# Optimization experiments

Hardware: AMD Instinct MI355X
Metric: run time of the kernel (lower is better)

The kernel has to match this reference:

```python
import jax, jax.numpy as jnp
import numpy as np

N_HEAD = 16
L_PARAM = 2  # module's L; min block = 2**L


def _build_sets(T, Lp):
    sets = []
    L = 2 ** Lp
    while L <= T:
        for i in range(T // L):
            sets.append((i * L, (i + 1) * L - 1))
        L *= 2
    return np.asarray(sets, dtype=np.int32)  # [nsets, 2]


def _get_slice(x_cum, l_idx, r_idx):
    # x_cum: [B, nh, T, hs]; returns cumulative-sum slice sums for each (l, r)
    r = x_cum[:, :, r_idx, :]
    l = x_cum[:, :, l_idx - 1, :] * (l_idx >= 1)[None, None, :, None]
    return r - l


def setup_inputs() -> dict:
    key = jax.random.key(0)
    k1, k2, k3 = jax.random.split(key, 3)
    B, T, C = 2, 2048, 1024
    x = jax.random.normal(k1, (B, T, C), dtype=jnp.float32)
    W_attn = jax.random.normal(k2, (3 * C, C), dtype=jnp.float32) * 0.02
    W_proj = jax.random.normal(k3, (C, C), dtype=jnp.float32) * 0.02
    return {"x": x, "W_attn": W_attn, "W_proj": W_proj}


def reference(x, W_attn, W_proj):
    B, T, C = x.shape
    nh, hs = N_HEAD, C // N_HEAD
    scale = 1.0 / np.sqrt(hs).astype(np.float32)

    qkv = x @ W_attn.T  # [B, T, 3C]
    q, k, v = jnp.split(qkv, 3, axis=2)
    q = q.reshape(B, T, nh, hs).transpose(0, 2, 1, 3)  # [B, nh, T, hs]
    k = k.reshape(B, T, nh, hs).transpose(0, 2, 1, 3)
    v = v.reshape(B, T, nh, hs).transpose(0, 2, 1, 3)

    # phi is identity, so q_phi = q, k_phi = k
    k_cum = jnp.cumsum(k, axis=2)
    v_cum = jnp.cumsum(v, axis=2)

    sets = _build_sets(T, L_PARAM)  # static, [nsets, 2]
    l_idx = jnp.asarray(sets[:, 0])
    r_idx = jnp.asarray(sets[:, 1])

    K = _get_slice(k_cum, l_idx, r_idx)  # [B, nh, nsets, hs]
    V = _get_slice(v_cum, l_idx, r_idx)

    t = jnp.arange(T)
    mask = t[:, None] >= r_idx[None, :]  # [T, nsets]

    att_logits = jnp.einsum('bhtd,bhsd->bhts', q, K) * scale
    att_logits = jnp.where(mask[None, None], att_logits, -jnp.inf)

    # tail term: remaining t % 2**L + 1 keys for each query
    Lmin = 2 ** L_PARAM
    tail_len = t % Lmin + 1
    l_tail = t - tail_len + 1
    K_tail = _get_slice(k_cum, l_tail, t)  # [B, nh, T, hs]
    V_tail = _get_slice(v_cum, l_tail, t)
    att_tail = jnp.sum(q * K_tail, axis=-1) * scale  # [B, nh, T]

    logits = jnp.concatenate([att_logits, att_tail[..., None]], axis=-1)
    att = jax.nn.softmax(logits, axis=-1)

    out = jnp.einsum('bhts,bhsd->bhtd', att[..., :-1], V) + att[..., -1:] * V_tail
    out = out.transpose(0, 2, 1, 3).reshape(B, T, C)
    return out @ W_proj.T
```

## Files before the change

kernel.cpp:

```cpp
#include <hip/hip_runtime.h>

typedef _Float16 f16x8 __attribute__((ext_vector_type(8)));
typedef unsigned short u16x8 __attribute__((ext_vector_type(8)));
typedef float f32x4  __attribute__((ext_vector_type(4)));
typedef unsigned short u16;

#define T_SEQ 2048
#define C_DIM 1024
#define NH 16
#define HS 64
#define S_SETS 1023
#define S_PAD 1024
#define SCALE 0.125f
#define NEG_BIG -1e30f

#define GLB(p) ((const __attribute__((address_space(1))) void*)(p))
#define LDS(p) ((__attribute__((address_space(3))) void*)(p))

__device__ __forceinline__ u16 f2h(float f) {
    _Float16 h = (_Float16)f;
    return __builtin_bit_cast(unsigned short, h);
}
__device__ __forceinline__ float h2f(u16 u) {
    _Float16 h = __builtin_bit_cast(_Float16, u);
    return (float)h;
}
__device__ __forceinline__ f32x4 mfmah(f16x8 a, f16x8 b, f32x4 c) {
    return __builtin_amdgcn_mfma_f32_16x16x32_f16(a, b, c, 0, 0, 0);
}

__global__ __launch_bounds__(256) void conv_f16(const float* __restrict__ in,
                                                u16* __restrict__ out, int n4) {
    int i = blockIdx.x * 256 + threadIdx.x;
    if (i >= n4) return;
    float4 f = ((const float4*)in)[i];
    ushort4 o;
    o.x = f2h(f.x); o.y = f2h(f.y); o.z = f2h(f.z); o.w = f2h(f.w);
    ((ushort4*)out)[i] = o;
}

__global__ __launch_bounds__(256) void gemm_qkv16(const u16* __restrict__ x16,
                                                  const u16* __restrict__ wa16,
                                                  u16* __restrict__ q16,
                                                  u16* __restrict__ k16,
                                                  u16* __restrict__ v16) {
    __shared__ u16 As[128 * 32];
    __shared__ u16 Bs[128 * 32];
    int tid = threadIdx.x, wv = tid >> 6, lane = tid & 63;
    int lm = lane & 15, quad = lane >> 4;
    int mt = blockIdx.x / 24, nt = blockIdx.x % 24;
    int wm = wv >> 1, wn = wv & 1;
    int m_off = wm * 64, n_off = wn * 64;

    const u16* gsrc;
    u16* ldst;
    int half = wv & 1;
    if (wv < 2) { gsrc = x16  + (size_t)(mt * 128 + half * 64) * C_DIM; ldst = As + half * 64 * 32; }
    else        { gsrc = wa16 + (size_t)(nt * 128 + half * 64) * C_DIM; ldst = Bs + half * 64 * 32; }
    int srow = lane >> 2, scol = (lane & 3) * 8;

    f32x4 acc[4][4];
    #pragma unroll
    for (int i = 0; i < 4; ++i)
        #pragma unroll
        for (int j = 0; j < 4; ++j) acc[i][j] = (f32x4){0.f, 0.f, 0.f, 0.f};

    for (int k0 = 0; k0 < C_DIM; k0 += 32) {
        __syncthreads();
        #pragma unroll
        for (int i = 0; i < 4; ++i) {
            int row = i * 16 + srow;
            __builtin_amdgcn_global_load_lds(
                GLB(gsrc + (size_t)row * C_DIM + k0 + scol),
                LDS(ldst + i * 512), 16, 0, 0);
        }
        __syncthreads();
        f16x8 af[4], bf[4];
        #pragma unroll
        for (int i = 0; i < 4; ++i) {
            af[i] = *(const f16x8*)(As + (m_off + i * 16 + lm) * 32 + quad * 8);
            bf[i] = *(const f16x8*)(Bs + (n_off + i * 16 + lm) * 32 + quad * 8);
        }
        #pragma unroll
        for (int mi = 0; mi < 4; ++mi)
            #pragma unroll
            for (int ni = 0; ni < 4; ++ni)
                acc[mi][ni] = mfmah(af[mi], bf[ni], acc[mi][ni]);
    }

    #pragma unroll
    for (int mi = 0; mi < 4; ++mi)
        #pragma unroll
        for (int ni = 0; ni < 4; ++ni) {
            int n = nt * 128 + n_off + ni * 16 + lm;
            int which = n >> 10, h = (n >> 6) & 15, d = n & 63;
            #pragma unroll
            for (int reg = 0; reg < 4; ++reg) {
                int m = mt * 128 + m_off + mi * 16 + quad * 4 + reg;
                int b_ = m >> 11, t = m & 2047;
                size_t oi = (((size_t)(b_ * NH + h)) * T_SEQ + t) * HS + d;
                float val = acc[mi][ni][reg];
                if (which == 0)      q16[oi] = f2h(val * SCALE);
                else if (which == 1) k16[oi] = f2h(val);
                else                 v16[oi] = f2h(val);
            }
        }
}

__global__ __launch_bounds__(256) void set_sums(const u16* __restrict__ k16,
                                                const u16* __restrict__ v16,
                                                u16* __restrict__ K16,
                                                u16* __restrict__ VT16) {
    int bh  = blockIdx.x;
    int src = blockIdx.y >> 2;
    int dc  = blockIdx.y & 3;
    int tid = threadIdx.x;
    __shared__ float lv0[512 * 16];
    __shared__ float lv1[256 * 16];
    const u16* sp = src ? v16 : k16;
    u16* op = src ? VT16 : K16;
    int dbase = dc * 16;
    for (int idx = tid; idx < 512 * 16; idx += 256) {
        int sg = idx >> 4, dd = idx & 15, d = dbase + dd;
        const u16* p = sp + ((size_t)bh * T_SEQ + sg * 4) * HS + d;
        float s = h2f(p[0]) + h2f(p[HS]) + h2f(p[2 * HS]) + h2f(p[3 * HS]);
        lv0[sg * 16 + dd] = s;
        size_t o = src ? ((size_t)bh * HS + d) * S_PAD + sg
                       : ((size_t)bh * S_PAD + sg) * HS + d;
        op[o] = f2h(s);
    }
    __syncthreads();
    int nsets = 256, offset = 512, lvl = 1;
    while (nsets >= 1) {
        float* sbuf = (lvl & 1) ? lv0 : lv1;
        float* dbuf = (lvl & 1) ? lv1 : lv0;
        for (int idx = tid; idx < nsets * 16; idx += 256) {
            int i = idx >> 4, dd = idx & 15, d = dbase + dd;
            float s = sbuf[(2 * i) * 16 + dd] + sbuf[(2 * i + 1) * 16 + dd];
            dbuf[i * 16 + dd] = s;
            int so = offset + i;
            size_t o = src ? ((size_t)bh * HS + d) * S_PAD + so
                           : ((size_t)bh * S_PAD + so) * HS + d;
            op[o] = f2h(s);
        }
        __syncthreads();
        offset += nsets; nsets >>= 1; lvl++;
    }
}

__global__ __launch_bounds__(256) void attn_flash16(const u16* __restrict__ q16,
                                                    const u16* __restrict__ k16,
                                                    const u16* __restrict__ v16,
                                                    const u16* __restrict__ K16,
                                                    const u16* __restrict__ VT16,
                                                    u16* __restrict__ att16) {
    int bh = blockIdx.y;
    int tid = threadIdx.x, wv = tid >> 6, lane = tid & 63;
    int lm = lane & 15, quad = lane >> 4;
    int tgrp = (wv < 2) ? (32 * blockIdx.x) : (2016 - 32 * blockIdx.x);
    int t0w = tgrp + (wv & 1) * 16;
    int twmax = t0w + 15;

    __shared__ u16 Ks[128 * 64];
    __shared__ u16 Pbuf[4][16 * 136];
    __shared__ float ptl[4][16];

    const u16* qg = q16 + ((size_t)bh * T_SEQ + t0w + lm) * HS;
    f16x8 a0 = *(const f16x8*)(qg + quad * 8);
    f16x8 a1 = *(const f16x8*)(qg + 32 + quad * 8);

    f32x4 O[4];
    #pragma unroll
    for (int i = 0; i < 4; ++i) O[i] = (f32x4){0.f, 0.f, 0.f, 0.f};
    f32x4 mrun = (f32x4){NEG_BIG, NEG_BIG, NEG_BIG, NEG_BIG};
    f32x4 lrun = (f32x4){0.f, 0.f, 0.f, 0.f};

    u16* Pw = &Pbuf[wv][0];
    const u16* vb = VT16 + (size_t)bh * HS * S_PAD;

    for (int c = 0; c < 8; ++c) {
        int s0 = c * 128;
        __syncthreads();
        {
            int row = tid >> 1, gb = (tid & 1) * 4, rx = row & 7;
            const u16* gk = K16 + ((size_t)bh * S_PAD + s0 + row) * HS;
            u16* dst = Ks + row * 64;
            #pragma unroll
            for (int uu = 0; uu < 4; ++uu) {
                int g = gb + uu;
                *(u16x8*)(dst + ((g ^ rx) << 3)) = *(const u16x8*)(gk + g * 8);
            }
        }
        __syncthreads();

        unsigned flags = 0;
        f32x4 lt[8];
        #pragma unroll
        for (int st = 0; st < 8; ++st) {
            int s = s0 + st * 16 + lm;
            bool sval = (s < S_SETS);
            int r = 0;
            if (sval) {
                int e = S_SETS - s;
                int l = __clz(e) - 22;
                int i0 = s - (1024 - (1024 >> l));
                r = (i0 + 1) * (4 << l) - 1;
            }
            unsigned long long bal = __ballot(sval && (r <= twmax));
            if (bal) {
                flags |= 1u << st;
                int sl = st * 16 + lm, sx = sl & 7;
                f16x8 b0 = *(const f16x8*)(Ks + sl * 64 + ((quad ^ sx) << 3));
                f16x8 b1 = *(const f16x8*)(Ks + sl * 64 + (((4 + quad) ^ sx) << 3));
                f32x4 a = (f32x4){0.f, 0.f, 0.f, 0.f};
                a = mfmah(a0, b0, a);
                a = mfmah(a1, b1, a);
                #pragma unroll
                for (int reg = 0; reg < 4; ++reg) {
                    int t = t0w + quad * 4 + reg;
                    lt[st][reg] = (sval && t >= r) ? a[reg] : NEG_BIG;
                }
            }
        }
        if (!flags) continue;

        f32x4 mc = (f32x4){NEG_BIG, NEG_BIG, NEG_BIG, NEG_BIG};
        #pragma unroll
        for (int st = 0; st < 8; ++st)
            if ((flags >> st) & 1u)
                #pragma unroll
                for (int reg = 0; reg < 4; ++reg) mc[reg] = fmaxf(mc[reg], lt[st][reg]);
        #pragma unroll
        for (int off = 1; off < 16; off <<= 1)
            #pragma unroll
            for (int reg = 0; reg < 4; ++reg)
                mc[reg] = fmaxf(mc[reg], __shfl_xor(mc[reg], off));
        f32x4 mnew, alpha, rs = (f32x4){0.f, 0.f, 0.f, 0.f};
        #pragma unroll
        for (int reg = 0; reg < 4; ++reg) {
            mnew[reg] = fmaxf(mrun[reg], mc[reg]);
            alpha[reg] = __expf(mrun[reg] - mnew[reg]);
        }
        #pragma unroll
        for (int st = 0; st < 8; ++st) {
            if ((flags >> st) & 1u) {
                #pragma unroll
                for (int reg = 0; reg < 4; ++reg) {
                    float lv = lt[st][reg];
                    float p = (lv > -5e29f) ? __expf(lv - mnew[reg]) : 0.f;
                    rs[reg] += p;
                    Pw[(quad * 4 + reg) * 136 + st * 16 + lm] = f2h(p);
                }
            } else {
                #pragma unroll
                for (int reg = 0; reg < 4; ++reg)
                    Pw[(quad * 4 + reg) * 136 + st * 16 + lm] = 0;
            }
        }
        #pragma unroll
        for (int off = 1; off < 16; off <<= 1)
            #pragma unroll
            for (int reg = 0; reg < 4; ++reg) rs[reg] += __shfl_xor(rs[reg], off);
        #pragma unroll
        for (int reg = 0; reg < 4; ++reg) {
            lrun[reg] = lrun[reg] * alpha[reg] + rs[reg];
            mrun[reg] = mnew[reg];
        }
        #pragma unroll
        for (int dt = 0; dt < 4; ++dt)
            #pragma unroll
            for (int reg = 0; reg < 4; ++reg) O[dt][reg] *= alpha[reg];

        #pragma unroll
        for (int kc = 0; kc < 4; ++kc) {
            if (!((flags >> (2 * kc)) & 3u)) continue;
            f16x8 afr = *(const f16x8*)(Pw + lm * 136 + kc * 32 + quad * 8);
            #pragma unroll
            for (int dt = 0; dt < 4; ++dt) {
                size_t vo = (size_t)(dt * 16 + lm) * S_PAD + s0 + kc * 32 + quad * 8;
                f16x8 bv = *(const f16x8*)(vb + vo);
                O[dt] = mfmah(afr, bv, O[dt]);
            }
        }
    }

    {
        int rqr = lane >> 2, prt = lane & 3;
        int tt = t0w + rqr;
        int lenr = (tt & 3) + 1;
        float ktv[16];
        #pragma unroll
        for (int dd = 0; dd < 16; ++dd) ktv[dd] = 0.f;
        for (int j = 0; j < lenr; ++j) {
            const u16* kp = k16 + ((size_t)bh * T_SEQ + tt - j) * HS + prt * 16;
            #pragma unroll
            for (int dd = 0; dd < 16; ++dd) ktv[dd] += h2f(kp[dd]);
        }
        const u16* tq = q16 + ((size_t)bh * T_SEQ + tt) * HS + prt * 16;
        float tlp = 0.f;
        #pragma unroll
        for (int dd = 0; dd < 16; ++dd) tlp += h2f(tq[dd]) * ktv[dd];
        tlp += __shfl_xor(tlp, 1);
        tlp += __shfl_xor(tlp, 2);
        if (prt == 0) ptl[wv][rqr] = tlp;
    }
    __syncthreads();

    int b_ = bh >> 4, h_ = bh & 15;
    #pragma unroll
    for (int reg = 0; reg < 4; ++reg) {
        int row = quad * 4 + reg;
        int t = t0w + row;
        float tl = ptl[wv][row];
        float mfin = fmaxf(mrun[reg], tl);
        float pt = __expf(tl - mfin);
        float af = __expf(mrun[reg] - mfin);
        float inv = 1.0f / (lrun[reg] * af + pt);
        int len = (t & 3) + 1;
        #pragma unroll
        for (int dt = 0; dt < 4; ++dt) {
            int d = dt * 16 + lm;
            const u16* vp = v16 + ((size_t)bh * T_SEQ + t) * HS + d;
            float vt = 0.f;
            for (int j = 0; j < len; ++j) vt += h2f(vp[-(j * HS)]);
            float val = (O[dt][reg] * af + pt * vt) * inv;
            att16[((size_t)(b_ * T_SEQ + t)) * C_DIM + h_ * HS + d] = f2h(val);
        }
    }
}

__global__ __launch_bounds__(256) void gemm_proj16(const u16* __restrict__ a_,
                                                   const u16* __restrict__ w,
                                                   float* __restrict__ out) {
    __shared__ u16 As[128 * 32];
    __shared__ u16 Bs[128 * 32];
    int tid = threadIdx.x, wv = tid >> 6, lane = tid & 63;
    int lm = lane & 15, quad = lane >> 4;
    int mt = blockIdx.x >> 3, nt = blockIdx.x & 7;
    int wm = wv >> 1, wn = wv & 1;
    int m_off = wm * 64, n_off = wn * 64;

    const u16* gsrc;
    u16* ldst;
    int half = wv & 1;
    if (wv < 2) { gsrc = a_ + (size_t)(mt * 128 + half * 64) * C_DIM; ldst = As + half * 64 * 32; }
    else        { gsrc = w  + (size_t)(nt * 128 + half * 64) * C_DIM; ldst = Bs + half * 64 * 32; }
    int srow = lane >> 2, scol = (lane & 3) * 8;

    f32x4 acc[4][4];
    #pragma unroll
    for (int i = 0; i < 4; ++i)
        #pragma unroll
        for (int j = 0; j < 4; ++j) acc[i][j] = (f32x4){0.f, 0.f, 0.f, 0.f};

    for (int k0 = 0; k0 < C_DIM; k0 += 32) {
        __syncthreads();
        #pragma unroll
        for (int i = 0; i < 4; ++i) {
            int row = i * 16 + srow;
            __builtin_amdgcn_global_load_lds(
                GLB(gsrc + (size_t)row * C_DIM + k0 + scol),
                LDS(ldst + i * 512), 16, 0, 0);
        }
        __syncthreads();
        f16x8 af[4], bf[4];
        #pragma unroll
        for (int i = 0; i < 4; ++i) {
            af[i] = *(const f16x8*)(As + (m_off + i * 16 + lm) * 32 + quad * 8);
            bf[i] = *(const f16x8*)(Bs + (n_off + i * 16 + lm) * 32 + quad * 8);
        }
        #pragma unroll
        for (int mi = 0; mi < 4; ++mi)
            #pragma unroll
            for (int ni = 0; ni < 4; ++ni)
                acc[mi][ni] = mfmah(af[mi], bf[ni], acc[mi][ni]);
    }

    #pragma unroll
    for (int mi = 0; mi < 4; ++mi)
        #pragma unroll
        for (int ni = 0; ni < 4; ++ni) {
            int n = nt * 128 + n_off + ni * 16 + lm;
            #pragma unroll
            for (int reg = 0; reg < 4; ++reg) {
                int m = mt * 128 + m_off + mi * 16 + quad * 4 + reg;
                out[(size_t)m * C_DIM + n] = acc[mi][ni][reg];
            }
        }
}

extern "C" void kernel_launch(void* const* d_in, const int* in_sizes, int n_in,
                              void* d_out, int out_size, void* d_ws, size_t ws_size,
                              hipStream_t stream) {
    const float* x     = (const float*)d_in[0];
    const float* Wattn = (const float*)d_in[1];
    const float* Wproj = (const float*)d_in[2];
    float* out = (float*)d_out;
    char* ws = (char*)d_ws;
    u16* x16   = (u16*)(ws + 0);
    u16* wa16  = (u16*)(ws + 8388608);
    u16* wp16  = (u16*)(ws + 14680064);
    u16* q16   = (u16*)(ws + 16777216);
    u16* k16   = (u16*)(ws + 25165824);
    u16* v16   = (u16*)(ws + 33554432);
    u16* K16   = (u16*)(ws + 41943040);
    u16* VT16  = (u16*)(ws + 46137344);
    u16* att16 = (u16*)(ws + 50331648);

    hipLaunchKernelGGL(conv_f16, dim3(4096), dim3(256), 0, stream, x, x16, 1048576);
    hipLaunchKernelGGL(conv_f16, dim3(3072), dim3(256), 0, stream, Wattn, wa16, 786432);
    hipLaunchKernelGGL(conv_f16, dim3(1024), dim3(256), 0, stream, Wproj, wp16, 262144);
    hipLaunchKernelGGL(gemm_qkv16, dim3(768), dim3(256), 0, stream, x16, wa16, q16, k16, v16);
    hipLaunchKernelGGL(set_sums, dim3(32, 8), dim3(256), 0, stream, k16, v16, K16, VT16);
    hipLaunchKernelGGL(attn_flash16, dim3(32, 32), dim3(256), 0, stream,
                       q16, k16, v16, K16, VT16, att16);
    hipLaunchKernelGGL(gemm_proj16, dim3(256), dim3(256), 0, stream, att16, wp16, out);
}
```

Before: 234.1 us.

## Split attention over set halves with LSE combine kernel and direct K loads

Splits the attention kernel's 1024 sets into two halves across a new grid dimension, each writing a normalized partial output and a log-sum-exp. A new combine kernel merges the two partials with the tail term. The per-chunk K tile staged in LDS is replaced by direct global loads, which removes two block barriers per chunk. Launch bounds now request 6 blocks per CU, and workspace buffers are reused. This is meant to raise parallelism and occupancy, at the cost of an extra kernel launch, extra partial-output traffic, and wasted work on the upper half where many queries see no valid sets.

Measured after the change: 346.4 us. 1.48x slower.

```diff
diff --git a/kernel.cpp b/kernel.cpp
--- a/kernel.cpp
+++ b/kernel.cpp
@@ -120,6 +120,12 @@
     const u16* sp = src ? v16 : k16;
     u16* op = src ? VT16 : K16;
     int dbase = dc * 16;
+    if (tid < 16) {
+        int d = dbase + tid;
+        size_t o = src ? ((size_t)bh * HS + d) * S_PAD + 1023
+                       : ((size_t)bh * S_PAD + 1023) * HS + d;
+        op[o] = 0;
+    }
     for (int idx = tid; idx < 512 * 16; idx += 256) {
         int sg = idx >> 4, dd = idx & 15, d = dbase + dd;
         const u16* p = sp + ((size_t)bh * T_SEQ + sg * 4) * HS + d;
@@ -148,22 +154,20 @@
     }
 }
 
-__global__ __launch_bounds__(256) void attn_flash16(const u16* __restrict__ q16,
-                                                    const u16* __restrict__ k16,
-                                                    const u16* __restrict__ v16,
-                                                    const u16* __restrict__ K16,
-                                                    const u16* __restrict__ VT16,
-                                                    u16* __restrict__ att16) {
+__global__ __launch_bounds__(256, 6) void attn_flash16(const u16* __restrict__ q16,
+                                                       const u16* __restrict__ K16,
+                                                       const u16* __restrict__ VT16,
+                                                       u16* __restrict__ Opart,
+                                                       float* __restrict__ LSEpart) {
     int bh = blockIdx.y;
+    int half = blockIdx.z;
     int tid = threadIdx.x, wv = tid >> 6, lane = tid & 63;
     int lm = lane & 15, quad = lane >> 4;
     int tgrp = (wv < 2) ? (32 * blockIdx.x) : (2016 - 32 * blockIdx.x);
     int t0w = tgrp + (wv & 1) * 16;
     int twmax = t0w + 15;
 
-    __shared__ u16 Ks[128 * 64];
-    __shared__ u16 Pbuf[4][16 * 136];
-    __shared__ float ptl[4][16];
+    __shared__ u16 Pbuf[4][16 * 72];
 
     const u16* qg = q16 + ((size_t)bh * T_SEQ + t0w + lm) * HS;
     f16x8 a0 = *(const f16x8*)(qg + quad * 8);
@@ -176,27 +180,16 @@
     f32x4 lrun = (f32x4){0.f, 0.f, 0.f, 0.f};
 
     u16* Pw = &Pbuf[wv][0];
-    const u16* vb = VT16 + (size_t)bh * HS * S_PAD;
+    const u16* vb  = VT16 + (size_t)bh * HS * S_PAD;
+    const u16* kbh = K16  + (size_t)bh * S_PAD * HS;
 
     for (int c = 0; c < 8; ++c) {
-        int s0 = c * 128;
-        __syncthreads();
-        {
-            int row = tid >> 1, gb = (tid & 1) * 4, rx = row & 7;
-            const u16* gk = K16 + ((size_t)bh * S_PAD + s0 + row) * HS;
-            u16* dst = Ks + row * 64;
-            #pragma unroll
-            for (int uu = 0; uu < 4; ++uu) {
-                int g = gb + uu;
-                *(u16x8*)(dst + ((g ^ rx) << 3)) = *(const u16x8*)(gk + g * 8);
-            }
-        }
-        __syncthreads();
+        int s0 = half * 512 + c * 64;
 
         unsigned flags = 0;
-        f32x4 lt[8];
-        #pragma unroll
-        for (int st = 0; st < 8; ++st) {
+        f32x4 lt[4];
+        #pragma unroll
+        for (int st = 0; st < 4; ++st) {
             int s = s0 + st * 16 + lm;
             bool sval = (s < S_SETS);
             int r = 0;
@@ -209,9 +202,9 @@
             unsigned long long bal = __ballot(sval && (r <= twmax));
             if (bal) {
                 flags |= 1u << st;
-                int sl = st * 16 + lm, sx = sl & 7;
-                f16x8 b0 = *(const f16x8*)(Ks + sl * 64 + ((quad ^ sx) << 3));
-                f16x8 b1 = *(const f16x8*)(Ks + sl * 64 + (((4 + quad) ^ sx) << 3));
+                const u16* kb = kbh + (size_t)(s0 + st * 16 + lm) * HS;
+                f16x8 b0 = *(const f16x8*)(kb + quad * 8);
+                f16x8 b1 = *(const f16x8*)(kb + 32 + quad * 8);
                 f32x4 a = (f32x4){0.f, 0.f, 0.f, 0.f};
                 a = mfmah(a0, b0, a);
                 a = mfmah(a1, b1, a);
@@ -226,7 +219,7 @@
 
         f32x4 mc = (f32x4){NEG_BIG, NEG_BIG, NEG_BIG, NEG_BIG};
         #pragma unroll
-        for (int st = 0; st < 8; ++st)
+        for (int st = 0; st < 4; ++st)
             if ((flags >> st) & 1u)
                 #pragma unroll
                 for (int reg = 0; reg < 4; ++reg) mc[reg] = fmaxf(mc[reg], lt[st][reg]);
@@ -242,19 +235,19 @@
             alpha[reg] = __expf(mrun[reg] - mnew[reg]);
         }
         #pragma unroll
-        for (int st = 0; st < 8; ++st) {
+        for (int st = 0; st < 4; ++st) {
             if ((flags >> st) & 1u) {
                 #pragma unroll
                 for (int reg = 0; reg < 4; ++reg) {
                     float lv = lt[st][reg];
                     float p = (lv > -5e29f) ? __expf(lv - mnew[reg]) : 0.f;
                     rs[reg] += p;
-                    Pw[(quad * 4 + reg) * 136 + st * 16 + lm] = f2h(p);
+                    Pw[(quad * 4 + reg) * 72 + st * 16 + lm] = f2h(p);
                 }
             } else {
                 #pragma unroll
                 for (int reg = 0; reg < 4; ++reg)
-                    Pw[(quad * 4 + reg) * 136 + st * 16 + lm] = 0;
+                    Pw[(quad * 4 + reg) * 72 + st * 16 + lm] = 0;
             }
         }
         #pragma unroll
@@ -272,9 +265,9 @@
             for (int reg = 0; reg < 4; ++reg) O[dt][reg] *= alpha[reg];
 
         #pragma unroll
-        for (int kc = 0; kc < 4; ++kc) {
+        for (int kc = 0; kc < 2; ++kc) {
             if (!((flags >> (2 * kc)) & 3u)) continue;
-            f16x8 afr = *(const f16x8*)(Pw + lm * 136 + kc * 32 + quad * 8);
+            f16x8 afr = *(const f16x8*)(Pw + lm * 72 + kc * 32 + quad * 8);
             #pragma unroll
             for (int dt = 0; dt < 4; ++dt) {
                 size_t vo = (size_t)(dt * 16 + lm) * S_PAD + s0 + kc * 32 + quad * 8;
@@ -284,49 +277,52 @@
         }
     }
 
-    {
-        int rqr = lane >> 2, prt = lane & 3;
-        int tt = t0w + rqr;
-        int lenr = (tt & 3) + 1;
-        float ktv[16];
-        #pragma unroll
-        for (int dd = 0; dd < 16; ++dd) ktv[dd] = 0.f;
-        for (int j = 0; j < lenr; ++j) {
-            const u16* kp = k16 + ((size_t)bh * T_SEQ + tt - j) * HS + prt * 16;
-            #pragma unroll
-            for (int dd = 0; dd < 16; ++dd) ktv[dd] += h2f(kp[dd]);
-        }
-        const u16* tq = q16 + ((size_t)bh * T_SEQ + tt) * HS + prt * 16;
-        float tlp = 0.f;
-        #pragma unroll
-        for (int dd = 0; dd < 16; ++dd) tlp += h2f(tq[dd]) * ktv[dd];
-        tlp += __shfl_xor(tlp, 1);
-        tlp += __shfl_xor(tlp, 2);
-        if (prt == 0) ptl[wv][rqr] = tlp;
-    }
-    __syncthreads();
+    u16* Ob = Opart + ((size_t)half * 32 + bh) * T_SEQ * HS;
+    float* Lb = LSEpart + ((size_t)half * 32 + bh) * T_SEQ;
+    #pragma unroll
+    for (int reg = 0; reg < 4; ++reg) {
+        int t = t0w + quad * 4 + reg;
+        float inv = lrun[reg] > 0.f ? 1.f / lrun[reg] : 0.f;
+        #pragma unroll
+        for (int dt = 0; dt < 4; ++dt)
+            Ob[(size_t)t * HS + dt * 16 + lm] = f2h(O[dt][reg] * inv);
+        if (lm == 0)
+            Lb[t] = lrun[reg] > 0.f ? mrun[reg] + __logf(lrun[reg]) : NEG_BIG;
+    }
+}
+
+__global__ __launch_bounds__(256) void attn_combine(const u16* __restrict__ q16,
+                                                    const u16* __restrict__ k16,
+                                                    const u16* __restrict__ v16,
+                                                    const u16* __restrict__ Opart,
+                                                    const float* __restrict__ LSEpart,
+                                                    u16* __restrict__ att16) {
+    int bh = blockIdx.y;
+    int wv = threadIdx.x >> 6, d = threadIdx.x & 63;
+    int t = blockIdx.x * 4 + wv;
+    size_t row = (size_t)bh * T_SEQ + t;
+
+    float lse0 = LSEpart[row];
+    float lse1 = LSEpart[(size_t)32 * T_SEQ + row];
+
+    int len = (t & 3) + 1;
+    const u16* kp = k16 + row * HS + d;
+    const u16* vp = v16 + row * HS + d;
+    float kt = 0.f, vt = 0.f;
+    for (int j = 0; j < len; ++j) { kt += h2f(kp[-j * HS]); vt += h2f(vp[-j * HS]); }
+    float tl = h2f(q16[row * HS + d]) * kt;
+    #pragma unroll
+    for (int off = 1; off < 64; off <<= 1) tl += __shfl_xor(tl, off);
+
+    float mf = fmaxf(fmaxf(lse0, lse1), tl);
+    float w0 = __expf(lse0 - mf), w1 = __expf(lse1 - mf), wt = __expf(tl - mf);
+    float inv = 1.f / (w0 + w1 + wt);
+    float o0 = h2f(Opart[row * HS + d]);
+    float o1 = h2f(Opart[(size_t)32 * T_SEQ * HS + row * HS + d]);
+    float val = (w0 * o0 + w1 * o1 + wt * vt) * inv;
 
     int b_ = bh >> 4, h_ = bh & 15;
-    #pragma unroll
-    for (int reg = 0; reg < 4; ++reg) {
-        int row = quad * 4 + reg;
-        int t = t0w + row;
-        float tl = ptl[wv][row];
-        float mfin = fmaxf(mrun[reg], tl);
-        float pt = __expf(tl - mfin);
-        float af = __expf(mrun[reg] - mfin);
-        float inv = 1.0f / (lrun[reg] * af + pt);
-        int len = (t & 3) + 1;
-        #pragma unroll
-        for (int dt = 0; dt < 4; ++dt) {
-            int d = dt * 16 + lm;
-            const u16* vp = v16 + ((size_t)bh * T_SEQ + t) * HS + d;
-            float vt = 0.f;
-            for (int j = 0; j < len; ++j) vt += h2f(vp[-(j * HS)]);
-            float val = (O[dt][reg] * af + pt * vt) * inv;
-            att16[((size_t)(b_ * T_SEQ + t)) * C_DIM + h_ * HS + d] = f2h(val);
-        }
-    }
+    att16[((size_t)b_ * T_SEQ + t) * C_DIM + h_ * HS + d] = f2h(val);
 }
 
 __global__ __launch_bounds__(256) void gemm_proj16(const u16* __restrict__ a_,
@@ -397,22 +393,26 @@
     const float* Wproj = (const float*)d_in[2];
     float* out = (float*)d_out;
     char* ws = (char*)d_ws;
-    u16* x16   = (u16*)(ws + 0);
-    u16* wa16  = (u16*)(ws + 8388608);
-    u16* wp16  = (u16*)(ws + 14680064);
-    u16* q16   = (u16*)(ws + 16777216);
-    u16* k16   = (u16*)(ws + 25165824);
-    u16* v16   = (u16*)(ws + 33554432);
-    u16* K16   = (u16*)(ws + 41943040);
-    u16* VT16  = (u16*)(ws + 46137344);
-    u16* att16 = (u16*)(ws + 50331648);
+    u16*  Opart = (u16*)(ws + 0);
+    u16*  x16   = (u16*)(ws + 0);
+    u16*  wa16  = (u16*)(ws + 8388608);
+    u16*  wp16  = (u16*)(ws + 0);
+    u16*  q16   = (u16*)(ws + 16777216);
+    u16*  k16   = (u16*)(ws + 25165824);
+    u16*  v16   = (u16*)(ws + 33554432);
+    u16*  K16   = (u16*)(ws + 41943040);
+    u16*  VT16  = (u16*)(ws + 46137344);
+    u16*  att16 = (u16*)(ws + 50331648);
+    float* LSE  = (float*)(ws + 58720256);
 
     hipLaunchKernelGGL(conv_f16, dim3(4096), dim3(256), 0, stream, x, x16, 1048576);
     hipLaunchKernelGGL(conv_f16, dim3(3072), dim3(256), 0, stream, Wattn, wa16, 786432);
-    hipLaunchKernelGGL(conv_f16, dim3(1024), dim3(256), 0, stream, Wproj, wp16, 262144);
     hipLaunchKernelGGL(gemm_qkv16, dim3(768), dim3(256), 0, stream, x16, wa16, q16, k16, v16);
     hipLaunchKernelGGL(set_sums, dim3(32, 8), dim3(256), 0, stream, k16, v16, K16, VT16);
-    hipLaunchKernelGGL(attn_flash16, dim3(32, 32), dim3(256), 0, stream,
-                       q16, k16, v16, K16, VT16, att16);
+    hipLaunchKernelGGL(attn_flash16, dim3(32, 32, 2), dim3(256), 0, stream,
+                       q16, K16, VT16, Opart, LSE);
+    hipLaunchKernelGGL(attn_combine, dim3(512, 32), dim3(256), 0, stream,
+                       q16, k16, v16, Opart, LSE, att16);
+    hipLaunchKernelGGL(conv_f16, dim3(1024), dim3(256), 0, stream, Wproj, wp16, 262144);
     hipLaunchKernelGGL(gemm_proj16, dim3(256), dim3(256), 0, stream, att16, wp16, out);
 }
```
